# Kernel tuning notes

Hardware: AMD Instinct MI355X
Metric: run time of the kernel (lower is better)

## Reference

```python
import jax, jax.numpy as jnp
import numpy as np

GAMMA = 1.0
NUM_CLASSES = 128


def setup_inputs() -> dict:
    key = jax.random.key(0)
    k1, k2, k3 = jax.random.split(key, 3)
    B, D, P = 8192, 512, 4096
    feature = jax.random.normal(k1, (B, D), dtype=jnp.float32)
    label = jax.random.randint(k2, (B,), 0, NUM_CLASSES)
    proto_features = jax.random.normal(k3, (P, D), dtype=jnp.float32)
    proto_labels = jnp.arange(P) % NUM_CLASSES  # every class has prototypes
    return {"feature": feature, "label": label,
            "proto_features": proto_features, "proto_labels": proto_labels}


def reference(feature, label, proto_features, proto_labels):
    # squared euclidean distances [B, P] via ||f||^2 + ||p||^2 - 2 f.p
    f_sq = jnp.sum(feature * feature, axis=-1, keepdims=True)          # [B,1]
    p_sq = jnp.sum(proto_features * proto_features, axis=-1)           # [P]
    d2 = f_sq + p_sq[None, :] - 2.0 * (feature @ proto_features.T)      # [B,P]
    d2 = jnp.maximum(d2, 0.0)
    logits = -GAMMA * d2                                                # [B,P]
    # denominator: sum over ALL prototypes; numerator: sum over own-class protos
    log_den = jax.scipy.special.logsumexp(logits, axis=-1)              # [B]
    same = proto_labels[None, :] == label[:, None]                      # [B,P]
    neg_inf = jnp.finfo(logits.dtype).min
    log_num = jax.scipy.special.logsumexp(
        jnp.where(same, logits, neg_inf), axis=-1)                      # [B]
    # loss = -log(num/den) per sample
    return log_den - log_num
```

## Files before the change

kernel.cpp:

```cpp
#include <hip/hip_runtime.h>
#include <hip/hip_bf16.h>

#define BN 8192
#define DK 512
#define PN 4096
#define GY 8
#define PPB 512
#define CH 32
#define NCH 16
#define STRIDE 520
#define SENT (-1.0e30f)
#define L2E 1.4426950408889634f
#define LN2 0.6931471805599453f

typedef __bf16 bf16x8 __attribute__((ext_vector_type(8)));
typedef float f32x4 __attribute__((ext_vector_type(4)));

__device__ __forceinline__ float ex2(float x) { return __builtin_amdgcn_exp2f(x); }

__device__ __forceinline__ void gl_lds16(const void* g, void* l) {
    __builtin_amdgcn_global_load_lds(
        (const __attribute__((address_space(1))) void*)g,
        (__attribute__((address_space(3))) void*)l, 16, 0, 0);
}

__global__ __launch_bounds__(256) void k_prep(const float* __restrict__ feat,
                                              const float* __restrict__ proto,
                                              __bf16* __restrict__ fB,
                                              __bf16* __restrict__ pB,
                                              float* __restrict__ p_sq) {
    int r  = blockIdx.x * 4 + (threadIdx.x >> 6);
    int ln = threadIdx.x & 63;
    if (r < PN) {
        const float* src = proto + (size_t)r * DK;
        float4 a = *(const float4*)(src + ln * 8);
        float4 b = *(const float4*)(src + ln * 8 + 4);
        float s = a.x * a.x + a.y * a.y + a.z * a.z + a.w * a.w
                + b.x * b.x + b.y * b.y + b.z * b.z + b.w * b.w;
#pragma unroll
        for (int m = 1; m < 64; m <<= 1) s += __shfl_xor(s, m, 64);
        int sidx = (r & 127) * 32 + (r >> 7);
        bf16x8 c;
        c[0] = (__bf16)a.x; c[1] = (__bf16)a.y; c[2] = (__bf16)a.z; c[3] = (__bf16)a.w;
        c[4] = (__bf16)b.x; c[5] = (__bf16)b.y; c[6] = (__bf16)b.z; c[7] = (__bf16)b.w;
        *(bf16x8*)(pB + (size_t)sidx * DK + ln * 8) = c;
        if (ln == 0) p_sq[sidx] = s * L2E;
    } else {
        int rf = r - PN;
        const float* src = feat + (size_t)rf * DK;
        float4 a = *(const float4*)(src + ln * 8);
        float4 b = *(const float4*)(src + ln * 8 + 4);
        bf16x8 c;
        c[0] = (__bf16)a.x; c[1] = (__bf16)a.y; c[2] = (__bf16)a.z; c[3] = (__bf16)a.w;
        c[4] = (__bf16)b.x; c[5] = (__bf16)b.y; c[6] = (__bf16)b.z; c[7] = (__bf16)b.w;
        *(bf16x8*)(fB + (size_t)rf * DK + ln * 8) = c;
    }
}

__global__ __launch_bounds__(256, 2) void k_main(
        const __bf16* __restrict__ fB,
        const __bf16* __restrict__ pB,
        const float* __restrict__ p_sq,
        const int* __restrict__ label,
        float4* __restrict__ part) {

    __shared__ __bf16 sM[2 * CH * STRIDE];
    __shared__ float  sPsq[PPB];

    const int t    = threadIdx.x;
    const int w    = t >> 6;
    const int l    = t & 63;
    const int ln   = l & 15;
    const int quad = l >> 4;
    const int bx   = blockIdx.x;
    const int gy   = blockIdx.y;
    const int rw   = bx * 128 + w * 32;
    const int p0   = gy * PPB;

    {
        const __bf16* g = pB + (size_t)(p0 + w * 8) * DK + l * 8;
        __bf16* lp = sM + (w * 8) * STRIDE;
#pragma unroll
        for (int j = 0; j < 8; ++j)
            gl_lds16(g + j * DK, lp + j * STRIDE);
    }

    bf16x8 afrag[2][16];
    {
        const __bf16* fb = fB + (size_t)(rw + ln) * DK + quad * 8;
#pragma unroll
        for (int mf = 0; mf < 2; ++mf)
#pragma unroll
            for (int ks = 0; ks < 16; ++ks)
                afrag[mf][ks] = *(const bf16x8*)(fb + (size_t)mf * 16 * DK + ks * 32);
    }

    int lab[2][4];
#pragma unroll
    for (int mf = 0; mf < 2; ++mf)
#pragma unroll
        for (int r = 0; r < 4; ++r)
            lab[mf][r] = label[rw + mf * 16 + quad * 4 + r];

    sPsq[t]       = p_sq[p0 + t];
    sPsq[t + 256] = p_sq[p0 + t + 256];
    __syncthreads();

    float Md[2][4], Sd[2][4], Mn[2][4], Sn[2][4];
#pragma unroll
    for (int mf = 0; mf < 2; ++mf)
#pragma unroll
        for (int r = 0; r < 4; ++r) {
            Md[mf][r] = SENT; Sd[mf][r] = 0.f;
            Mn[mf][r] = SENT; Sn[mf][r] = 0.f;
        }

#pragma unroll 1
    for (int nt = 0; nt < NCH; ++nt) {
        if (nt + 1 < NCH) {
            const __bf16* g = pB + (size_t)(p0 + (nt + 1) * CH + w * 8) * DK + l * 8;
            __bf16* lp = sM + (((nt + 1) & 1) * CH + w * 8) * STRIDE;
#pragma unroll
            for (int j = 0; j < 8; ++j)
                gl_lds16(g + j * DK, lp + j * STRIDE);
        }

        const __bf16* sB = sM + (nt & 1) * CH * STRIDE;

        f32x4 acc[2][2];
#pragma unroll
        for (int mf = 0; mf < 2; ++mf)
#pragma unroll
            for (int nf = 0; nf < 2; ++nf)
                acc[mf][nf] = (f32x4){0.f, 0.f, 0.f, 0.f};

#pragma unroll
        for (int ks = 0; ks < 16; ++ks) {
            bf16x8 b0 = *(const bf16x8*)(sB + ln * STRIDE + ks * 32 + quad * 8);
            bf16x8 b1 = *(const bf16x8*)(sB + (16 + ln) * STRIDE + ks * 32 + quad * 8);
            acc[0][0] = __builtin_amdgcn_mfma_f32_16x16x32_bf16(afrag[0][ks], b0, acc[0][0], 0, 0, 0);
            acc[0][1] = __builtin_amdgcn_mfma_f32_16x16x32_bf16(afrag[0][ks], b1, acc[0][1], 0, 0, 0);
            acc[1][0] = __builtin_amdgcn_mfma_f32_16x16x32_bf16(afrag[1][ks], b0, acc[1][0], 0, 0, 0);
            acc[1][1] = __builtin_amdgcn_mfma_f32_16x16x32_bf16(afrag[1][ks], b1, acc[1][1], 0, 0, 0);
        }

        float nps0 = -sPsq[nt * 32 + ln];
        float nps1 = -sPsq[nt * 32 + 16 + ln];
        const int cls = gy * 16 + nt;

        float z[2][2][4];
#pragma unroll
        for (int mf = 0; mf < 2; ++mf)
#pragma unroll
            for (int r = 0; r < 4; ++r) {
                z[mf][0][r] = fmaf(acc[mf][0][r], 2.0f * L2E, nps0);
                z[mf][1][r] = fmaf(acc[mf][1][r], 2.0f * L2E, nps1);
            }

#pragma unroll
        for (int mf = 0; mf < 2; ++mf)
#pragma unroll
            for (int r = 0; r < 4; ++r) {
                float z0 = z[mf][0][r], z1 = z[mf][1][r];
                float nm = fmaxf(Md[mf][r], fmaxf(z0, z1));
                float e  = ex2(z0 - nm) + ex2(z1 - nm);
                Sd[mf][r] = fmaf(Sd[mf][r], ex2(Md[mf][r] - nm), e);
                Md[mf][r] = nm;
            }

        int anyhit = 0;
#pragma unroll
        for (int mf = 0; mf < 2; ++mf)
#pragma unroll
            for (int r = 0; r < 4; ++r)
                anyhit |= (cls == lab[mf][r]);
        if (__any(anyhit)) {
#pragma unroll
            for (int mf = 0; mf < 2; ++mf)
#pragma unroll
                for (int r = 0; r < 4; ++r) {
                    bool hit = (cls == lab[mf][r]);
                    float z0 = z[mf][0][r], z1 = z[mf][1][r];
                    float nm = fmaxf(z0, z1);
                    float sn = ex2(z0 - nm) + ex2(z1 - nm);
                    Mn[mf][r] = hit ? nm : Mn[mf][r];
                    Sn[mf][r] = hit ? sn : Sn[mf][r];
                }
        }
        __syncthreads();
    }

#pragma unroll
    for (int mf = 0; mf < 2; ++mf)
#pragma unroll
        for (int r = 0; r < 4; ++r) {
            float md = Md[mf][r], sd = Sd[mf][r];
            float mn = Mn[mf][r], sn = Sn[mf][r];
#pragma unroll
            for (int m = 1; m < 16; m <<= 1) {
                float omd = __shfl_xor(md, m, 64);
                float osd = __shfl_xor(sd, m, 64);
                float omn = __shfl_xor(mn, m, 64);
                float osn = __shfl_xor(sn, m, 64);
                float nm = fmaxf(md, omd);
                sd = sd * ex2(md - nm) + osd * ex2(omd - nm);
                md = nm;
                nm = fmaxf(mn, omn);
                sn = sn * ex2(mn - nm) + osn * ex2(omn - nm);
                mn = nm;
            }
            if (ln == 0) {
                int row = rw + mf * 16 + quad * 4 + r;
                part[row * GY + gy] = make_float4(md, sd, mn, sn);
            }
        }
}

__global__ __launch_bounds__(256) void k_comb(const float4* __restrict__ part,
                                              float* __restrict__ out) {
    int row = blockIdx.x * 256 + threadIdx.x;
    float md = SENT, sd = 0.f, mn = SENT, sn = 0.f;
#pragma unroll
    for (int q = 0; q < GY; ++q) {
        float4 v = part[row * GY + q];
        float nm = fmaxf(md, v.x);
        sd = sd * ex2(md - nm) + v.y * ex2(v.x - nm);
        md = nm;
        nm = fmaxf(mn, v.z);
        sn = sn * ex2(mn - nm) + v.w * ex2(v.z - nm);
        mn = nm;
    }
    out[row] = ((md + __builtin_amdgcn_logf(sd)) - (mn + __builtin_amdgcn_logf(sn))) * LN2;
}

extern "C" void kernel_launch(void* const* d_in, const int* in_sizes, int n_in,
                              void* d_out, int out_size, void* d_ws, size_t ws_size,
                              hipStream_t stream) {
    const float* feat   = (const float*)d_in[0];
    const int*   label  = (const int*)d_in[1];
    const float* proto  = (const float*)d_in[2];
    float*       out    = (float*)d_out;

    char* w = (char*)d_ws;
    __bf16* fB    = (__bf16*)(w);
    __bf16* pB    = (__bf16*)(w + 8388608);
    float*  p_sq  = (float*)(w + 12582912);
    float4* part  = (float4*)(w + 12599296);

    hipLaunchKernelGGL(k_prep, dim3((PN + BN) / 4), dim3(256), 0, stream,
                       feat, proto, fB, pB, p_sq);
    hipLaunchKernelGGL(k_main, dim3(64, GY), dim3(256), 0, stream,
                       fB, pB, p_sq, label, part);
    hipLaunchKernelGGL(k_comb, dim3(BN / 256), dim3(256), 0, stream,
                       part, out);
}
```

Measured before the change: 118.9 us.

## Shrink per-wave tile to 16x16 and raise occupancy in main kernel

Each wave now covers 16 feature rows against 16-prototype chunks, down from 32 rows against 32 prototypes. The grid doubles along the batch dimension and the launch bound asks for 4 blocks per CU to gain occupancy and latency hiding. Because a class now spans two chunks, the own-class numerator is accumulated with an online max/sum instead of being overwritten per chunk. The trade-offs are less operand reuse (one LDS B read per MFMA), twice the global prototype traffic, and more exp2 calls per logit in the running denominator update.

```diff
diff --git a/kernel.cpp b/kernel.cpp
--- a/kernel.cpp
+++ b/kernel.cpp
@@ -6,8 +6,8 @@
 #define PN 4096
 #define GY 8
 #define PPB 512
-#define CH 32
-#define NCH 16
+#define CH 16
+#define NCH 32
 #define STRIDE 520
 #define SENT (-1.0e30f)
 #define L2E 1.4426950408889634f
@@ -57,7 +57,7 @@
     }
 }
 
-__global__ __launch_bounds__(256, 2) void k_main(
+__global__ __launch_bounds__(256, 4) void k_main(
         const __bf16* __restrict__ fB,
         const __bf16* __restrict__ pB,
         const float* __restrict__ p_sq,
@@ -74,146 +74,107 @@
     const int quad = l >> 4;
     const int bx   = blockIdx.x;
     const int gy   = blockIdx.y;
-    const int rw   = bx * 128 + w * 32;
+    const int rw   = bx * 64 + w * 16;
     const int p0   = gy * PPB;
 
     {
-        const __bf16* g = pB + (size_t)(p0 + w * 8) * DK + l * 8;
-        __bf16* lp = sM + (w * 8) * STRIDE;
-#pragma unroll
-        for (int j = 0; j < 8; ++j)
+        const __bf16* g = pB + (size_t)(p0 + w * 4) * DK + l * 8;
+        __bf16* lp = sM + (w * 4) * STRIDE;
+#pragma unroll
+        for (int j = 0; j < 4; ++j)
             gl_lds16(g + j * DK, lp + j * STRIDE);
     }
 
-    bf16x8 afrag[2][16];
+    bf16x8 afrag[16];
     {
         const __bf16* fb = fB + (size_t)(rw + ln) * DK + quad * 8;
 #pragma unroll
-        for (int mf = 0; mf < 2; ++mf)
-#pragma unroll
-            for (int ks = 0; ks < 16; ++ks)
-                afrag[mf][ks] = *(const bf16x8*)(fb + (size_t)mf * 16 * DK + ks * 32);
-    }
-
-    int lab[2][4];
-#pragma unroll
-    for (int mf = 0; mf < 2; ++mf)
-#pragma unroll
-        for (int r = 0; r < 4; ++r)
-            lab[mf][r] = label[rw + mf * 16 + quad * 4 + r];
+        for (int ks = 0; ks < 16; ++ks)
+            afrag[ks] = *(const bf16x8*)(fb + ks * 32);
+    }
+
+    int lab[4];
+#pragma unroll
+    for (int r = 0; r < 4; ++r)
+        lab[r] = label[rw + quad * 4 + r];
 
     sPsq[t]       = p_sq[p0 + t];
     sPsq[t + 256] = p_sq[p0 + t + 256];
     __syncthreads();
 
-    float Md[2][4], Sd[2][4], Mn[2][4], Sn[2][4];
-#pragma unroll
-    for (int mf = 0; mf < 2; ++mf)
-#pragma unroll
-        for (int r = 0; r < 4; ++r) {
-            Md[mf][r] = SENT; Sd[mf][r] = 0.f;
-            Mn[mf][r] = SENT; Sn[mf][r] = 0.f;
-        }
+    float Md[4], Sd[4], Mn[4], Sn[4];
+#pragma unroll
+    for (int r = 0; r < 4; ++r) {
+        Md[r] = SENT; Sd[r] = 0.f;
+        Mn[r] = SENT; Sn[r] = 0.f;
+    }
 
 #pragma unroll 1
     for (int nt = 0; nt < NCH; ++nt) {
         if (nt + 1 < NCH) {
-            const __bf16* g = pB + (size_t)(p0 + (nt + 1) * CH + w * 8) * DK + l * 8;
-            __bf16* lp = sM + (((nt + 1) & 1) * CH + w * 8) * STRIDE;
-#pragma unroll
-            for (int j = 0; j < 8; ++j)
+            const __bf16* g = pB + (size_t)(p0 + (nt + 1) * CH + w * 4) * DK + l * 8;
+            __bf16* lp = sM + (((nt + 1) & 1) * CH + w * 4) * STRIDE;
+#pragma unroll
+            for (int j = 0; j < 4; ++j)
                 gl_lds16(g + j * DK, lp + j * STRIDE);
         }
 
         const __bf16* sB = sM + (nt & 1) * CH * STRIDE;
 
-        f32x4 acc[2][2];
-#pragma unroll
-        for (int mf = 0; mf < 2; ++mf)
-#pragma unroll
-            for (int nf = 0; nf < 2; ++nf)
-                acc[mf][nf] = (f32x4){0.f, 0.f, 0.f, 0.f};
-
+        f32x4 acc = (f32x4){0.f, 0.f, 0.f, 0.f};
 #pragma unroll
         for (int ks = 0; ks < 16; ++ks) {
             bf16x8 b0 = *(const bf16x8*)(sB + ln * STRIDE + ks * 32 + quad * 8);
-            bf16x8 b1 = *(const bf16x8*)(sB + (16 + ln) * STRIDE + ks * 32 + quad * 8);
-            acc[0][0] = __builtin_amdgcn_mfma_f32_16x16x32_bf16(afrag[0][ks], b0, acc[0][0], 0, 0, 0);
-            acc[0][1] = __builtin_amdgcn_mfma_f32_16x16x32_bf16(afrag[0][ks], b1, acc[0][1], 0, 0, 0);
-            acc[1][0] = __builtin_amdgcn_mfma_f32_16x16x32_bf16(afrag[1][ks], b0, acc[1][0], 0, 0, 0);
-            acc[1][1] = __builtin_amdgcn_mfma_f32_16x16x32_bf16(afrag[1][ks], b1, acc[1][1], 0, 0, 0);
-        }
-
-        float nps0 = -sPsq[nt * 32 + ln];
-        float nps1 = -sPsq[nt * 32 + 16 + ln];
-        const int cls = gy * 16 + nt;
-
-        float z[2][2][4];
-#pragma unroll
-        for (int mf = 0; mf < 2; ++mf)
-#pragma unroll
-            for (int r = 0; r < 4; ++r) {
-                z[mf][0][r] = fmaf(acc[mf][0][r], 2.0f * L2E, nps0);
-                z[mf][1][r] = fmaf(acc[mf][1][r], 2.0f * L2E, nps1);
+            acc = __builtin_amdgcn_mfma_f32_16x16x32_bf16(afrag[ks], b0, acc, 0, 0, 0);
+        }
+
+        float nps = -sPsq[nt * CH + ln];
+        const int cls = gy * 16 + (nt >> 1);
+
+        int anyhit = 0;
+#pragma unroll
+        for (int r = 0; r < 4; ++r)
+            anyhit |= (cls == lab[r]);
+        bool dohit = __any(anyhit);
+
+#pragma unroll
+        for (int r = 0; r < 4; ++r) {
+            float z  = fmaf(acc[r], 2.0f * L2E, nps);
+            float nm = fmaxf(Md[r], z);
+            Sd[r] = fmaf(Sd[r], ex2(Md[r] - nm), ex2(z - nm));
+            Md[r] = nm;
+            if (dohit) {
+                float zn = (cls == lab[r]) ? z : SENT;
+                float n2 = fmaxf(Mn[r], zn);
+                Sn[r] = fmaf(Sn[r], ex2(Mn[r] - n2), ex2(zn - n2));
+                Mn[r] = n2;
             }
-
-#pragma unroll
-        for (int mf = 0; mf < 2; ++mf)
-#pragma unroll
-            for (int r = 0; r < 4; ++r) {
-                float z0 = z[mf][0][r], z1 = z[mf][1][r];
-                float nm = fmaxf(Md[mf][r], fmaxf(z0, z1));
-                float e  = ex2(z0 - nm) + ex2(z1 - nm);
-                Sd[mf][r] = fmaf(Sd[mf][r], ex2(Md[mf][r] - nm), e);
-                Md[mf][r] = nm;
-            }
-
-        int anyhit = 0;
-#pragma unroll
-        for (int mf = 0; mf < 2; ++mf)
-#pragma unroll
-            for (int r = 0; r < 4; ++r)
-                anyhit |= (cls == lab[mf][r]);
-        if (__any(anyhit)) {
-#pragma unroll
-            for (int mf = 0; mf < 2; ++mf)
-#pragma unroll
-                for (int r = 0; r < 4; ++r) {
-                    bool hit = (cls == lab[mf][r]);
-                    float z0 = z[mf][0][r], z1 = z[mf][1][r];
-                    float nm = fmaxf(z0, z1);
-                    float sn = ex2(z0 - nm) + ex2(z1 - nm);
-                    Mn[mf][r] = hit ? nm : Mn[mf][r];
-                    Sn[mf][r] = hit ? sn : Sn[mf][r];
-                }
         }
         __syncthreads();
     }
 
 #pragma unroll
-    for (int mf = 0; mf < 2; ++mf)
-#pragma unroll
-        for (int r = 0; r < 4; ++r) {
-            float md = Md[mf][r], sd = Sd[mf][r];
-            float mn = Mn[mf][r], sn = Sn[mf][r];
-#pragma unroll
-            for (int m = 1; m < 16; m <<= 1) {
-                float omd = __shfl_xor(md, m, 64);
-                float osd = __shfl_xor(sd, m, 64);
-                float omn = __shfl_xor(mn, m, 64);
-                float osn = __shfl_xor(sn, m, 64);
-                float nm = fmaxf(md, omd);
-                sd = sd * ex2(md - nm) + osd * ex2(omd - nm);
-                md = nm;
-                nm = fmaxf(mn, omn);
-                sn = sn * ex2(mn - nm) + osn * ex2(omn - nm);
-                mn = nm;
-            }
-            if (ln == 0) {
-                int row = rw + mf * 16 + quad * 4 + r;
-                part[row * GY + gy] = make_float4(md, sd, mn, sn);
-            }
-        }
+    for (int r = 0; r < 4; ++r) {
+        float md = Md[r], sd = Sd[r];
+        float mn = Mn[r], sn = Sn[r];
+#pragma unroll
+        for (int m = 1; m < 16; m <<= 1) {
+            float omd = __shfl_xor(md, m, 64);
+            float osd = __shfl_xor(sd, m, 64);
+            float omn = __shfl_xor(mn, m, 64);
+            float osn = __shfl_xor(sn, m, 64);
+            float nm = fmaxf(md, omd);
+            sd = sd * ex2(md - nm) + osd * ex2(omd - nm);
+            md = nm;
+            nm = fmaxf(mn, omn);
+            sn = sn * ex2(mn - nm) + osn * ex2(omn - nm);
+            mn = nm;
+        }
+        if (ln == 0) {
+            int row = rw + quad * 4 + r;
+            part[row * GY + gy] = make_float4(md, sd, mn, sn);
+        }
+    }
 }
 
 __global__ __launch_bounds__(256) void k_comb(const float4* __restrict__ part,
@@ -249,7 +210,7 @@
 
     hipLaunchKernelGGL(k_prep, dim3((PN + BN) / 4), dim3(256), 0, stream,
                        feat, proto, fB, pB, p_sq);
-    hipLaunchKernelGGL(k_main, dim3(64, GY), dim3(256), 0, stream,
+    hipLaunchKernelGGL(k_main, dim3(128, GY), dim3(256), 0, stream,
                        fB, pB, p_sq, label, part);
     hipLaunchKernelGGL(k_comb, dim3(BN / 256), dim3(256), 0, stream,
                        part, out);
```

New measurement: 131.4 us. 10.5% more time.
